# Performance work log

Measured on AMD Instinct MI355X. Metric: run time of the kernel, lower is better.

The kernel has to match this reference:

```python
import jax, jax.numpy as jnp
import numpy as np

N_HEAD = 16
ROPE_BASE = 10000.0


def _rope_tables(T, head_dim, dtype):
    inv_freq = 1.0 / (ROPE_BASE ** (jnp.arange(0, head_dim, 2, dtype=jnp.float32) / head_dim))
    t = jnp.arange(T, dtype=jnp.float32)
    freqs = t[:, None] * inv_freq[None, :]          # [T, hd/2]
    emb = jnp.concatenate([freqs, freqs], axis=-1)  # [T, hd]
    return jnp.cos(emb).astype(dtype), jnp.sin(emb).astype(dtype)


def _rotate_half(x):
    h = x.shape[-1] // 2
    return jnp.concatenate([-x[..., h:], x[..., :h]], axis=-1)


def setup_inputs() -> dict:
    key = jax.random.key(0)
    k1, k2, k3 = jax.random.split(key, 3)
    B, T, C = 2, 2048, 1024
    x = jax.random.normal(k1, (B, T, C), dtype=jnp.float32)
    w_attn = jax.random.normal(k2, (3 * C, C), dtype=jnp.float32) * (1.0 / np.sqrt(C))
    w_proj = jax.random.normal(k3, (C, C), dtype=jnp.float32) * (1.0 / np.sqrt(C))
    return {"x": x, "w_attn": w_attn, "w_proj": w_proj}


def reference(x, w_attn, w_proj):
    B, T, C = x.shape
    H = N_HEAD
    hd = C // H

    qkv = jnp.einsum('btc,fc->btf', x, w_attn)          # [B,T,3C]
    q, k, v = jnp.split(qkv, 3, axis=-1)
    # [B,H,T,hd]
    q = q.reshape(B, T, H, hd).transpose(0, 2, 1, 3)
    k = k.reshape(B, T, H, hd).transpose(0, 2, 1, 3)
    v = v.reshape(B, T, H, hd).transpose(0, 2, 1, 3)

    cos, sin = _rope_tables(T, hd, x.dtype)             # [T,hd]
    cos = cos[None, None]
    sin = sin[None, None]
    q = q * cos + _rotate_half(q) * sin
    k = k * cos + _rotate_half(k) * sin

    scale = 1.0 / np.sqrt(hd)
    scores = jnp.einsum('bhqd,bhkd->bhqk', q, k) * scale  # [B,H,T,T]
    causal = jnp.tril(jnp.ones((T, T), dtype=bool))
    scores = jnp.where(causal[None, None], scores, jnp.finfo(scores.dtype).min)
    attn = jax.nn.softmax(scores, axis=-1)
    out = jnp.einsum('bhqk,bhkd->bhqd', attn, v)          # [B,H,T,hd]
    out = out.transpose(0, 2, 1, 3).reshape(B, T, C)
    return jnp.einsum('btc,oc->bto', out, w_proj)
```

## Files before the change

### kernel.cpp

```cpp
#include <hip/hip_runtime.h>
#include <hip/hip_bf16.h>
#include <stdint.h>

typedef unsigned short u16;
typedef __bf16 bf16x8 __attribute__((ext_vector_type(8)));
typedef float f32x4 __attribute__((ext_vector_type(4)));

#define B_ 2
#define T_ 2048
#define C_ 1024
#define H_ 16
#define HD 64
#define M_ (B_ * T_)
#define N3 (3 * C_)

#define WAITV(N) asm volatile("s_waitcnt vmcnt(" #N ")" ::: "memory")

__device__ __forceinline__ float bf2f(u16 u) {
  return __uint_as_float(((unsigned int)u) << 16);
}
__device__ __forceinline__ u16 f2bf(float f) {
  unsigned int u = __float_as_uint(f);
  u += 0x7FFF + ((u >> 16) & 1);
  return (u16)(u >> 16);
}
__device__ __forceinline__ unsigned cvt_pk_bf16(float lo, float hi) {
  unsigned r;
  asm("v_cvt_pk_bf16_f32 %0, %1, %2" : "=v"(r) : "v"(lo), "v"(hi));
  return r;
}
__device__ __forceinline__ void async16(void* ldsp, const void* gp) {
  __builtin_amdgcn_global_load_lds(
      (const __attribute__((address_space(1))) unsigned int*)gp,
      (__attribute__((address_space(3))) unsigned int*)ldsp, 16, 0, 0);
}

union U16x8 { uint4 v; u16 u[8]; };

__device__ __forceinline__ bf16x8 ldsAfrag(const char* base, int row, int kbyte) {
  int off = (row * 128 + kbyte) ^ ((row & 7) << 4);
  uint4 t = *reinterpret_cast<const uint4*>(base + off);
  return __builtin_bit_cast(bf16x8, t);
}
__device__ __forceinline__ bf16x8 ldsRead(const char* p) {
  uint4 t = *reinterpret_cast<const uint4*>(p);
  return __builtin_bit_cast(bf16x8, t);
}

__global__ void cvt_bf16(const float* __restrict__ src, u16* __restrict__ dst, int n4) {
  int i = blockIdx.x * blockDim.x + threadIdx.x;
  int stride = gridDim.x * blockDim.x;
  for (; i < n4; i += stride) {
    float4 v = reinterpret_cast<const float4*>(src)[i];
    uint2 o;
    o.x = (unsigned)f2bf(v.x) | ((unsigned)f2bf(v.y) << 16);
    o.y = (unsigned)f2bf(v.z) | ((unsigned)f2bf(v.w) << 16);
    reinterpret_cast<uint2*>(dst)[i] = o;
  }
}

__global__ void rope_tables_kernel(float* __restrict__ cosT, float* __restrict__ sinT) {
  int t = blockIdx.x;
  int i = threadIdx.x;
  float inv = powf(10000.0f, -(float)i * (1.0f / 32.0f));
  float f = (float)t * inv;
  cosT[t * 32 + i] = cosf(f);
  sinT[t * 32 + i] = sinf(f);
}

template <bool OUT_F32>
__global__ __launch_bounds__(256) void gemm_bt(const u16* __restrict__ A,
                                               const u16* __restrict__ Bw,
                                               void* __restrict__ Cout,
                                               int M, int N, int K) {
  __shared__ uint4 ldsbuf[2048];
  char* As = (char*)ldsbuf;
  char* Bs = (char*)ldsbuf + 16384;
  const int tid = threadIdx.x;
  const int lane = tid & 63;
  const int wv = tid >> 6;
  const int wr = wv >> 1, wc = wv & 1;
  const int lrow = lane & 15, lgrp = lane >> 4;
  const long m0 = (long)blockIdx.x * 128, n0 = (long)blockIdx.y * 128;
  const int srow_l = lane >> 3;
  const int csrc = ((lane & 7) ^ (lane >> 3)) * 8;
  f32x4 acc[4][4] = {};
  for (int k0 = 0; k0 < K; k0 += 64) {
    __syncthreads();
#pragma unroll
    for (int p = 0; p < 4; ++p) {
      int seg = wv * 4 + p;
      int row = seg * 8 + srow_l;
      async16(As + seg * 1024, A + (size_t)(m0 + row) * K + k0 + csrc);
      async16(Bs + seg * 1024, Bw + (size_t)(n0 + row) * K + k0 + csrc);
    }
    __syncthreads();
#pragma unroll
    for (int ks = 0; ks < 2; ++ks) {
      bf16x8 af[4], bfr[4];
#pragma unroll
      for (int i = 0; i < 4; ++i) {
        af[i]  = ldsAfrag(As, wr * 64 + i * 16 + lrow, ks * 64 + lgrp * 16);
        bfr[i] = ldsAfrag(Bs, wc * 64 + i * 16 + lrow, ks * 64 + lgrp * 16);
      }
#pragma unroll
      for (int i = 0; i < 4; ++i)
#pragma unroll
        for (int j = 0; j < 4; ++j)
          acc[i][j] = __builtin_amdgcn_mfma_f32_16x16x32_bf16(af[i], bfr[j], acc[i][j], 0, 0, 0);
    }
  }
#pragma unroll
  for (int i = 0; i < 4; ++i)
#pragma unroll
    for (int j = 0; j < 4; ++j) {
      long r0 = m0 + wr * 64 + i * 16 + lgrp * 4;
      long c  = n0 + wc * 64 + j * 16 + lrow;
#pragma unroll
      for (int r = 0; r < 4; ++r) {
        float v = acc[i][j][r];
        if (OUT_F32)
          ((float*)Cout)[(r0 + r) * N + c] = v;
        else
          ((u16*)Cout)[(r0 + r) * N + c] = f2bf(v);
      }
    }
}

__global__ __launch_bounds__(256) void rope_reshape(const u16* __restrict__ qkv,
                                                    const float* __restrict__ cosT,
                                                    const float* __restrict__ sinT,
                                                    u16* __restrict__ Q,
                                                    u16* __restrict__ K,
                                                    u16* __restrict__ Vt) {
  __shared__ u16 Vs[64][80];
  const float SCLQ = 0.125f * 1.4426950408889634f;
  const int tid = threadIdx.x;
  const int tblk = blockIdx.x, bh = blockIdx.y;
  const int b = bh >> 4, h = bh & 15;
  const int tl = tid >> 2, quar = tid & 3;
  const int t = tblk * 64 + tl;
  const u16* rowp = qkv + ((size_t)(b * T_ + t)) * N3 + h * HD;
  const int d0 = quar * 8;
  float cs[8], sn[8];
#pragma unroll
  for (int j = 0; j < 8; ++j) {
    cs[j] = cosT[t * 32 + d0 + j];
    sn[j] = sinT[t * 32 + d0 + j];
  }
#pragma unroll
  for (int part = 0; part < 2; ++part) {
    const u16* p = rowp + part * C_;
    U16x8 x1, x2, o1, o2;
    x1.v = *reinterpret_cast<const uint4*>(p + d0);
    x2.v = *reinterpret_cast<const uint4*>(p + d0 + 32);
#pragma unroll
    for (int j = 0; j < 8; ++j) {
      float a = bf2f(x1.u[j]), c2 = bf2f(x2.u[j]);
      float f1 = a * cs[j] - c2 * sn[j];
      float f2 = c2 * cs[j] + a * sn[j];
      if (part == 0) { f1 *= SCLQ; f2 *= SCLQ; }
      o1.u[j] = f2bf(f1);
      o2.u[j] = f2bf(f2);
    }
    u16* dst = (part ? K : Q) + ((size_t)bh * T_ + t) * HD;
    *reinterpret_cast<uint4*>(dst + d0) = o1.v;
    *reinterpret_cast<uint4*>(dst + d0 + 32) = o2.v;
  }
  const u16* pv = rowp + 2 * C_;
#pragma unroll
  for (int c = 0; c < 2; ++c) {
    int d = quar * 16 + c * 8;
    *reinterpret_cast<uint4*>(&Vs[tl][d]) = *reinterpret_cast<const uint4*>(pv + d);
  }
  __syncthreads();
  const int d = tid >> 2, tq = tid & 3;
  U16x8 a, bv;
#pragma unroll
  for (int j = 0; j < 8; ++j) a.u[j] = Vs[tq * 16 + j][d];
#pragma unroll
  for (int j = 0; j < 8; ++j) bv.u[j] = Vs[tq * 16 + 8 + j][d];
  u16* dstv = Vt + ((size_t)bh * HD + d) * T_ + tblk * 64 + tq * 16;
  *reinterpret_cast<uint4*>(dstv) = a.v;
  *reinterpret_cast<uint4*>(dstv + 8) = bv.v;
}

__global__ __launch_bounds__(256) void attn_fwd9(const u16* __restrict__ Q,
                                                 const u16* __restrict__ K,
                                                 const u16* __restrict__ Vt,
                                                 u16* __restrict__ O) {
  __shared__ uint4 lds4[4608];
  char* ldsb = (char*)lds4;
  const int tid = threadIdx.x;
  const int lane = tid & 63, wv = tid >> 6;
  const int lrow = lane & 15, lgrp = lane >> 4;
  const int bh = blockIdx.y;
  const int b = bh >> 4, h = bh & 15;
  const u16* Qh = Q + (size_t)bh * T_ * HD;
  const u16* Kh = K + (size_t)bh * T_ * HD;
  const u16* Vh = Vt + (size_t)bh * HD * T_;

  const int srow_l = lane >> 3;
  const int csrc = ((lane & 7) ^ (lane >> 3)) * 8;

  auto stage = [&](int slot, int kt) {
    char* Kd = ldsb + (slot << 14);
    char* Vd = Kd + 8192;
    const u16* Kg = Kh + (size_t)(kt * 64) * HD;
    const u16* Vg = Vh + kt * 64;
#pragma unroll
    for (int seg = 0; seg < 2; ++seg) {
      int row = wv * 16 + seg * 8 + srow_l;
      async16(Kd + wv * 2048 + seg * 1024, Kg + (size_t)row * HD + csrc);
      async16(Vd + wv * 2048 + seg * 1024, Vg + (size_t)row * T_ + csrc);
    }
  };

  const int swz = (lrow & 7) << 4;
  const int krA = lrow * 128 + ((lgrp * 16) ^ swz);
  const int krB = lrow * 128 + ((64 + lgrp * 16) ^ swz);
  const int vrA = 8192 + krA;
  const int vrB = 8192 + krB;
  char* PsW = ldsb + 65536 + wv * 2048 + lrow * 128;
  char* pw0 = PsW + ((0 * 32 + lgrp * 8) ^ swz);
  char* pw1 = PsW + ((1 * 32 + lgrp * 8) ^ swz);
  char* pw2 = PsW + ((2 * 32 + lgrp * 8) ^ swz);
  char* pw3 = PsW + ((3 * 32 + lgrp * 8) ^ swz);
  const char* paA = PsW + ((lgrp * 16) ^ swz);
  const char* paB = PsW + ((64 + lgrp * 16) ^ swz);

  uint4 ones4;
  ones4.x = ones4.y = ones4.z = ones4.w = 0x3F803F80u;
  const bf16x8 ones8 = __builtin_bit_cast(bf16x8, ones4);

#pragma unroll
  for (int uu = 0; uu < 2; ++uu) {
    const int unit = uu ? (31 - (int)blockIdx.x) : (int)blockIdx.x;
    const int qs = unit * 64;
    const int q_glob = qs + wv * 16 + lrow;
    const int nu = unit + 1;

    bf16x8 qf[2];
#pragma unroll
    for (int ks = 0; ks < 2; ++ks) {
      uint4 t4 = *reinterpret_cast<const uint4*>(
          Qh + (size_t)(qs + wv * 16 + lrow) * HD + ks * 32 + lgrp * 8);
      qf[ks] = __builtin_bit_cast(bf16x8, t4);
    }
    f32x4 o[4] = {};
    f32x4 lacc = {};

    {
      const int pre = nu < 3 ? nu : 3;
      for (int i = 0; i < pre; ++i) stage(i, i);
      WAITV(0);
      __builtin_amdgcn_s_barrier();
      __builtin_amdgcn_sched_barrier(0);
    }

    for (int kt = 0; kt < nu; ++kt) {
      if (kt + 3 < nu) stage((kt + 3) & 3, kt + 3);
      const char* buf = ldsb + ((kt & 3) << 14);
      const char* KbA = buf + krA;
      const char* KbB = buf + krB;
      const char* VbA = buf + vrA;
      const char* VbB = buf + vrB;

      f32x4 s[4] = {};
      __builtin_amdgcn_s_setprio(1);
#pragma unroll
      for (int n = 0; n < 4; ++n)
        s[n] = __builtin_amdgcn_mfma_f32_16x16x32_bf16(ldsRead(KbA + n * 2048), qf[0], s[n], 0, 0, 0);
#pragma unroll
      for (int n = 0; n < 4; ++n)
        s[n] = __builtin_amdgcn_mfma_f32_16x16x32_bf16(ldsRead(KbB + n * 2048), qf[1], s[n], 0, 0, 0);
      __builtin_amdgcn_s_setprio(0);

      if (kt == nu - 1) {
#pragma unroll
        for (int n = 0; n < 4; ++n)
#pragma unroll
          for (int r = 0; r < 4; ++r) {
            int kg = kt * 64 + n * 16 + lgrp * 4 + r;
            float v = (kg <= q_glob) ? s[n][r] : -__builtin_inff();
            s[n][r] = exp2f(v);
          }
      } else {
#pragma unroll
        for (int n = 0; n < 4; ++n)
#pragma unroll
          for (int r = 0; r < 4; ++r) s[n][r] = exp2f(s[n][r]);
      }

      {
        uint2 w0, w1, w2, w3;
        w0.x = cvt_pk_bf16(s[0][0], s[0][1]); w0.y = cvt_pk_bf16(s[0][2], s[0][3]);
        w1.x = cvt_pk_bf16(s[1][0], s[1][1]); w1.y = cvt_pk_bf16(s[1][2], s[1][3]);
        w2.x = cvt_pk_bf16(s[2][0], s[2][1]); w2.y = cvt_pk_bf16(s[2][2], s[2][3]);
        w3.x = cvt_pk_bf16(s[3][0], s[3][1]); w3.y = cvt_pk_bf16(s[3][2], s[3][3]);
        *reinterpret_cast<uint2*>(pw0) = w0;
        *reinterpret_cast<uint2*>(pw1) = w1;
        *reinterpret_cast<uint2*>(pw2) = w2;
        *reinterpret_cast<uint2*>(pw3) = w3;
      }

      __builtin_amdgcn_s_setprio(1);
#pragma unroll
      for (int ks = 0; ks < 2; ++ks) {
        bf16x8 pa = ldsRead(ks ? paB : paA);
        lacc = __builtin_amdgcn_mfma_f32_16x16x32_bf16(pa, ones8, lacc, 0, 0, 0);
        const char* vbb = ks ? VbB : VbA;
#pragma unroll
        for (int dn = 0; dn < 4; ++dn) {
          bf16x8 bv = ldsRead(vbb + dn * 2048);
          o[dn] = __builtin_amdgcn_mfma_f32_16x16x32_bf16(pa, bv, o[dn], 0, 0, 0);
        }
      }
      __builtin_amdgcn_s_setprio(0);

      if (kt + 4 <= nu)      WAITV(8);
      else if (kt + 3 == nu) WAITV(4);
      else                   WAITV(0);
      __builtin_amdgcn_s_barrier();
      __builtin_amdgcn_sched_barrier(0);
    }

#pragma unroll
    for (int r = 0; r < 4; ++r) {
      float inv = 1.0f / lacc[r];
      int t = qs + wv * 16 + lgrp * 4 + r;
#pragma unroll
      for (int dn = 0; dn < 4; ++dn) {
        int c = h * HD + dn * 16 + lrow;
        O[((size_t)(b * T_ + t)) * C_ + c] = f2bf(o[dn][r] * inv);
      }
    }
  }
}

extern "C" void kernel_launch(void* const* d_in, const int* in_sizes, int n_in,
                              void* d_out, int out_size, void* d_ws, size_t ws_size,
                              hipStream_t stream) {
  const float* x  = (const float*)d_in[0];
  const float* wa = (const float*)d_in[1];
  const float* wp = (const float*)d_in[2];
  float* out = (float*)d_out;
  char* ws = (char*)d_ws;
  size_t off = 0;
  auto alloc = [&](size_t bytes) {
    char* p = ws + off;
    off += (bytes + 255) & ~(size_t)255;
    return p;
  };
  u16* xb   = (u16*)alloc((size_t)M_ * C_ * 2);
  u16* wab  = (u16*)alloc((size_t)N3 * C_ * 2);
  u16* wpb  = (u16*)alloc((size_t)C_ * C_ * 2);
  u16* qkvb = (u16*)alloc((size_t)M_ * N3 * 2);
  u16* Qb   = (u16*)alloc((size_t)B_ * H_ * T_ * HD * 2);
  u16* Kb   = (u16*)alloc((size_t)B_ * H_ * T_ * HD * 2);
  u16* Vtb  = (u16*)alloc((size_t)B_ * H_ * T_ * HD * 2);
  u16* Ob   = (u16*)alloc((size_t)M_ * C_ * 2);
  float* cosT = (float*)alloc((size_t)T_ * 32 * 4);
  float* sinT = (float*)alloc((size_t)T_ * 32 * 4);
  (void)in_sizes; (void)n_in; (void)out_size; (void)ws_size;

  cvt_bf16<<<1024, 256, 0, stream>>>(x, xb, M_ * C_ / 4);
  cvt_bf16<<<1024, 256, 0, stream>>>(wa, wab, N3 * C_ / 4);
  cvt_bf16<<<512, 256, 0, stream>>>(wp, wpb, C_ * C_ / 4);
  rope_tables_kernel<<<T_, 32, 0, stream>>>(cosT, sinT);
  gemm_bt<false><<<dim3(M_ / 128, N3 / 128), 256, 0, stream>>>(xb, wab, qkvb, M_, N3, C_);
  rope_reshape<<<dim3(T_ / 64, B_ * H_), 256, 0, stream>>>(qkvb, cosT, sinT, Qb, Kb, Vtb);
  attn_fwd9<<<dim3(16, B_ * H_), 256, 0, stream>>>(Qb, Kb, Vtb, Ob);
  gemm_bt<true><<<dim3(M_ / 128, C_ / 128), 256, 0, stream>>>(Ob, wpb, out, M_, C_, C_);
}
```

Baseline: 128.7 us.

## Read K/V fragments directly from global memory in attention, one q-tile per block

```diff
diff --git a/kernel.cpp b/kernel.cpp
--- a/kernel.cpp
+++ b/kernel.cpp
@@ -14,8 +14,6 @@
 #define M_ (B_ * T_)
 #define N3 (3 * C_)
 
-#define WAITV(N) asm volatile("s_waitcnt vmcnt(" #N ")" ::: "memory")
-
 __device__ __forceinline__ float bf2f(u16 u) {
   return __uint_as_float(((unsigned int)u) << 16);
 }
@@ -43,6 +41,10 @@
   return __builtin_bit_cast(bf16x8, t);
 }
 __device__ __forceinline__ bf16x8 ldsRead(const char* p) {
+  uint4 t = *reinterpret_cast<const uint4*>(p);
+  return __builtin_bit_cast(bf16x8, t);
+}
+__device__ __forceinline__ bf16x8 gRead(const char* p) {
   uint4 t = *reinterpret_cast<const uint4*>(p);
   return __builtin_bit_cast(bf16x8, t);
 }
@@ -185,43 +187,25 @@
   *reinterpret_cast<uint4*>(dstv + 8) = bv.v;
 }
 
-__global__ __launch_bounds__(256) void attn_fwd9(const u16* __restrict__ Q,
-                                                 const u16* __restrict__ K,
-                                                 const u16* __restrict__ Vt,
-                                                 u16* __restrict__ O) {
-  __shared__ uint4 lds4[4608];
-  char* ldsb = (char*)lds4;
+__global__ __launch_bounds__(256) void attn_fwd10(const u16* __restrict__ Q,
+                                                  const u16* __restrict__ K,
+                                                  const u16* __restrict__ Vt,
+                                                  u16* __restrict__ O) {
+  __shared__ char Plds[8192];
   const int tid = threadIdx.x;
   const int lane = tid & 63, wv = tid >> 6;
   const int lrow = lane & 15, lgrp = lane >> 4;
   const int bh = blockIdx.y;
   const int b = bh >> 4, h = bh & 15;
   const u16* Qh = Q + (size_t)bh * T_ * HD;
-  const u16* Kh = K + (size_t)bh * T_ * HD;
-  const u16* Vh = Vt + (size_t)bh * HD * T_;
-
-  const int srow_l = lane >> 3;
-  const int csrc = ((lane & 7) ^ (lane >> 3)) * 8;
-
-  auto stage = [&](int slot, int kt) {
-    char* Kd = ldsb + (slot << 14);
-    char* Vd = Kd + 8192;
-    const u16* Kg = Kh + (size_t)(kt * 64) * HD;
-    const u16* Vg = Vh + kt * 64;
-#pragma unroll
-    for (int seg = 0; seg < 2; ++seg) {
-      int row = wv * 16 + seg * 8 + srow_l;
-      async16(Kd + wv * 2048 + seg * 1024, Kg + (size_t)row * HD + csrc);
-      async16(Vd + wv * 2048 + seg * 1024, Vg + (size_t)row * T_ + csrc);
-    }
-  };
+  const char* Kb = (const char*)(K + (size_t)bh * T_ * HD);
+  const char* Vb = (const char*)(Vt + (size_t)bh * HD * T_);
+
+  const char* kbase = Kb + lrow * 128 + lgrp * 16;
+  const char* vbase = Vb + lrow * 4096 + lgrp * 16;
 
   const int swz = (lrow & 7) << 4;
-  const int krA = lrow * 128 + ((lgrp * 16) ^ swz);
-  const int krB = lrow * 128 + ((64 + lgrp * 16) ^ swz);
-  const int vrA = 8192 + krA;
-  const int vrB = 8192 + krB;
-  char* PsW = ldsb + 65536 + wv * 2048 + lrow * 128;
+  char* PsW = Plds + wv * 2048 + lrow * 128;
   char* pw0 = PsW + ((0 * 32 + lgrp * 8) ^ swz);
   char* pw1 = PsW + ((1 * 32 + lgrp * 8) ^ swz);
   char* pw2 = PsW + ((2 * 32 + lgrp * 8) ^ swz);
@@ -233,107 +217,86 @@
   ones4.x = ones4.y = ones4.z = ones4.w = 0x3F803F80u;
   const bf16x8 ones8 = __builtin_bit_cast(bf16x8, ones4);
 
-#pragma unroll
-  for (int uu = 0; uu < 2; ++uu) {
-    const int unit = uu ? (31 - (int)blockIdx.x) : (int)blockIdx.x;
-    const int qs = unit * 64;
-    const int q_glob = qs + wv * 16 + lrow;
-    const int nu = unit + 1;
-
-    bf16x8 qf[2];
+  const int unit = 31 - (int)blockIdx.x;
+  const int qs = unit * 64;
+  const int q_glob = qs + wv * 16 + lrow;
+  const int nu = unit + 1;
+
+  bf16x8 qf[2];
+#pragma unroll
+  for (int ks = 0; ks < 2; ++ks) {
+    uint4 t4 = *reinterpret_cast<const uint4*>(
+        Qh + (size_t)(qs + wv * 16 + lrow) * HD + ks * 32 + lgrp * 8);
+    qf[ks] = __builtin_bit_cast(bf16x8, t4);
+  }
+  f32x4 o[4] = {};
+  f32x4 lacc = {};
+
+  for (int kt = 0; kt < nu; ++kt) {
+    const char* kp = kbase + (size_t)kt * 8192;
+
+    f32x4 s[4] = {};
+    __builtin_amdgcn_s_setprio(1);
+#pragma unroll
+    for (int n = 0; n < 4; ++n) {
+      bf16x8 f0 = gRead(kp + n * 2048);
+      bf16x8 f1 = gRead(kp + n * 2048 + 64);
+      s[n] = __builtin_amdgcn_mfma_f32_16x16x32_bf16(f0, qf[0], s[n], 0, 0, 0);
+      s[n] = __builtin_amdgcn_mfma_f32_16x16x32_bf16(f1, qf[1], s[n], 0, 0, 0);
+    }
+    __builtin_amdgcn_s_setprio(0);
+
+    if (kt == nu - 1) {
+#pragma unroll
+      for (int n = 0; n < 4; ++n)
+#pragma unroll
+        for (int r = 0; r < 4; ++r) {
+          int kg = kt * 64 + n * 16 + lgrp * 4 + r;
+          float v = (kg <= q_glob) ? s[n][r] : -__builtin_inff();
+          s[n][r] = exp2f(v);
+        }
+    } else {
+#pragma unroll
+      for (int n = 0; n < 4; ++n)
+#pragma unroll
+        for (int r = 0; r < 4; ++r) s[n][r] = exp2f(s[n][r]);
+    }
+
+    {
+      uint2 w0, w1, w2, w3;
+      w0.x = cvt_pk_bf16(s[0][0], s[0][1]); w0.y = cvt_pk_bf16(s[0][2], s[0][3]);
+      w1.x = cvt_pk_bf16(s[1][0], s[1][1]); w1.y = cvt_pk_bf16(s[1][2], s[1][3]);
+      w2.x = cvt_pk_bf16(s[2][0], s[2][1]); w2.y = cvt_pk_bf16(s[2][2], s[2][3]);
+      w3.x = cvt_pk_bf16(s[3][0], s[3][1]); w3.y = cvt_pk_bf16(s[3][2], s[3][3]);
+      *reinterpret_cast<uint2*>(pw0) = w0;
+      *reinterpret_cast<uint2*>(pw1) = w1;
+      *reinterpret_cast<uint2*>(pw2) = w2;
+      *reinterpret_cast<uint2*>(pw3) = w3;
+    }
+
+    const char* vp = vbase + (size_t)kt * 128;
+    __builtin_amdgcn_s_setprio(1);
 #pragma unroll
     for (int ks = 0; ks < 2; ++ks) {
-      uint4 t4 = *reinterpret_cast<const uint4*>(
-          Qh + (size_t)(qs + wv * 16 + lrow) * HD + ks * 32 + lgrp * 8);
-      qf[ks] = __builtin_bit_cast(bf16x8, t4);
-    }
-    f32x4 o[4] = {};
-    f32x4 lacc = {};
-
-    {
-      const int pre = nu < 3 ? nu : 3;
-      for (int i = 0; i < pre; ++i) stage(i, i);
-      WAITV(0);
-      __builtin_amdgcn_s_barrier();
-      __builtin_amdgcn_sched_barrier(0);
-    }
-
-    for (int kt = 0; kt < nu; ++kt) {
-      if (kt + 3 < nu) stage((kt + 3) & 3, kt + 3);
-      const char* buf = ldsb + ((kt & 3) << 14);
-      const char* KbA = buf + krA;
-      const char* KbB = buf + krB;
-      const char* VbA = buf + vrA;
-      const char* VbB = buf + vrB;
-
-      f32x4 s[4] = {};
-      __builtin_amdgcn_s_setprio(1);
-#pragma unroll
-      for (int n = 0; n < 4; ++n)
-        s[n] = __builtin_amdgcn_mfma_f32_16x16x32_bf16(ldsRead(KbA + n * 2048), qf[0], s[n], 0, 0, 0);
-#pragma unroll
-      for (int n = 0; n < 4; ++n)
-        s[n] = __builtin_amdgcn_mfma_f32_16x16x32_bf16(ldsRead(KbB + n * 2048), qf[1], s[n], 0, 0, 0);
-      __builtin_amdgcn_s_setprio(0);
-
-      if (kt == nu - 1) {
-#pragma unroll
-        for (int n = 0; n < 4; ++n)
-#pragma unroll
-          for (int r = 0; r < 4; ++r) {
-            int kg = kt * 64 + n * 16 + lgrp * 4 + r;
-            float v = (kg <= q_glob) ? s[n][r] : -__builtin_inff();
-            s[n][r] = exp2f(v);
-          }
-      } else {
-#pragma unroll
-        for (int n = 0; n < 4; ++n)
-#pragma unroll
-          for (int r = 0; r < 4; ++r) s[n][r] = exp2f(s[n][r]);
+      bf16x8 pa = ldsRead(ks ? paB : paA);
+      lacc = __builtin_amdgcn_mfma_f32_16x16x32_bf16(pa, ones8, lacc, 0, 0, 0);
+#pragma unroll
+      for (int dn = 0; dn < 4; ++dn) {
+        bf16x8 bv = gRead(vp + dn * 65536 + ks * 64);
+        o[dn] = __builtin_amdgcn_mfma_f32_16x16x32_bf16(pa, bv, o[dn], 0, 0, 0);
       }
-
-      {
-        uint2 w0, w1, w2, w3;
-        w0.x = cvt_pk_bf16(s[0][0], s[0][1]); w0.y = cvt_pk_bf16(s[0][2], s[0][3]);
-        w1.x = cvt_pk_bf16(s[1][0], s[1][1]); w1.y = cvt_pk_bf16(s[1][2], s[1][3]);
-        w2.x = cvt_pk_bf16(s[2][0], s[2][1]); w2.y = cvt_pk_bf16(s[2][2], s[2][3]);
-        w3.x = cvt_pk_bf16(s[3][0], s[3][1]); w3.y = cvt_pk_bf16(s[3][2], s[3][3]);
-        *reinterpret_cast<uint2*>(pw0) = w0;
-        *reinterpret_cast<uint2*>(pw1) = w1;
-        *reinterpret_cast<uint2*>(pw2) = w2;
-        *reinterpret_cast<uint2*>(pw3) = w3;
-      }
-
-      __builtin_amdgcn_s_setprio(1);
-#pragma unroll
-      for (int ks = 0; ks < 2; ++ks) {
-        bf16x8 pa = ldsRead(ks ? paB : paA);
-        lacc = __builtin_amdgcn_mfma_f32_16x16x32_bf16(pa, ones8, lacc, 0, 0, 0);
-        const char* vbb = ks ? VbB : VbA;
-#pragma unroll
-        for (int dn = 0; dn < 4; ++dn) {
-          bf16x8 bv = ldsRead(vbb + dn * 2048);
-          o[dn] = __builtin_amdgcn_mfma_f32_16x16x32_bf16(pa, bv, o[dn], 0, 0, 0);
-        }
-      }
-      __builtin_amdgcn_s_setprio(0);
-
-      if (kt + 4 <= nu)      WAITV(8);
-      else if (kt + 3 == nu) WAITV(4);
-      else                   WAITV(0);
-      __builtin_amdgcn_s_barrier();
-      __builtin_amdgcn_sched_barrier(0);
-    }
-
-#pragma unroll
-    for (int r = 0; r < 4; ++r) {
-      float inv = 1.0f / lacc[r];
-      int t = qs + wv * 16 + lgrp * 4 + r;
-#pragma unroll
-      for (int dn = 0; dn < 4; ++dn) {
-        int c = h * HD + dn * 16 + lrow;
-        O[((size_t)(b * T_ + t)) * C_ + c] = f2bf(o[dn][r] * inv);
-      }
+    }
+    __builtin_amdgcn_s_setprio(0);
+  }
+
+#pragma unroll
+  for (int r = 0; r < 4; ++r) {
+    float inv = 1.0f / lacc[r];
+    int t = qs + wv * 16 + lgrp * 4 + r;
+#pragma unroll
+    for (int dn = 0; dn < 4; ++dn) {
+      int c = h * HD + dn * 16 + lrow;
+      O[((size_t)(b * T_ + t)) * C_ + c] = f2bf(o[dn][r] * inv);
     }
   }
 }
@@ -370,6 +333,6 @@
   rope_tables_kernel<<<T_, 32, 0, stream>>>(cosT, sinT);
   gemm_bt<false><<<dim3(M_ / 128, N3 / 128), 256, 0, stream>>>(xb, wab, qkvb, M_, N3, C_);
   rope_reshape<<<dim3(T_ / 64, B_ * H_), 256, 0, stream>>>(qkvb, cosT, sinT, Qb, Kb, Vtb);
-  attn_fwd9<<<dim3(16, B_ * H_), 256, 0, stream>>>(Qb, Kb, Vtb, Ob);
+  attn_fwd10<<<dim3(32, B_ * H_), 256, 0, stream>>>(Qb, Kb, Vtb, Ob);
   gemm_bt<true><<<dim3(M_ / 128, C_ / 128), 256, 0, stream>>>(Ob, wpb, out, M_, C_, C_);
 }
```

Result: slower. 304.8 us (+136.8%).

## Split paired causal units into separate blocks with double-buffered LDS staging

Applied to the files above, without the earlier changes.

```diff
diff --git a/kernel.cpp b/kernel.cpp
--- a/kernel.cpp
+++ b/kernel.cpp
@@ -13,8 +13,6 @@
 #define HD 64
 #define M_ (B_ * T_)
 #define N3 (3 * C_)
-
-#define WAITV(N) asm volatile("s_waitcnt vmcnt(" #N ")" ::: "memory")
 
 __device__ __forceinline__ float bf2f(u16 u) {
   return __uint_as_float(((unsigned int)u) << 16);
@@ -185,11 +183,11 @@
   *reinterpret_cast<uint4*>(dstv + 8) = bv.v;
 }
 
-__global__ __launch_bounds__(256) void attn_fwd9(const u16* __restrict__ Q,
-                                                 const u16* __restrict__ K,
-                                                 const u16* __restrict__ Vt,
-                                                 u16* __restrict__ O) {
-  __shared__ uint4 lds4[4608];
+__global__ __launch_bounds__(256) void attn_fwd11(const u16* __restrict__ Q,
+                                                  const u16* __restrict__ K,
+                                                  const u16* __restrict__ Vt,
+                                                  u16* __restrict__ O) {
+  __shared__ uint4 lds4[2560];
   char* ldsb = (char*)lds4;
   const int tid = threadIdx.x;
   const int lane = tid & 63, wv = tid >> 6;
@@ -221,7 +219,7 @@
   const int krB = lrow * 128 + ((64 + lgrp * 16) ^ swz);
   const int vrA = 8192 + krA;
   const int vrB = 8192 + krB;
-  char* PsW = ldsb + 65536 + wv * 2048 + lrow * 128;
+  char* PsW = ldsb + 32768 + wv * 2048 + lrow * 128;
   char* pw0 = PsW + ((0 * 32 + lgrp * 8) ^ swz);
   char* pw1 = PsW + ((1 * 32 + lgrp * 8) ^ swz);
   char* pw2 = PsW + ((2 * 32 + lgrp * 8) ^ swz);
@@ -233,107 +231,96 @@
   ones4.x = ones4.y = ones4.z = ones4.w = 0x3F803F80u;
   const bf16x8 ones8 = __builtin_bit_cast(bf16x8, ones4);
 
-#pragma unroll
-  for (int uu = 0; uu < 2; ++uu) {
-    const int unit = uu ? (31 - (int)blockIdx.x) : (int)blockIdx.x;
-    const int qs = unit * 64;
-    const int q_glob = qs + wv * 16 + lrow;
-    const int nu = unit + 1;
-
-    bf16x8 qf[2];
+  const int unit = 31 - (int)blockIdx.x;
+  const int qs = unit * 64;
+  const int q_glob = qs + wv * 16 + lrow;
+  const int nu = unit + 1;
+
+  bf16x8 qf[2];
+#pragma unroll
+  for (int ks = 0; ks < 2; ++ks) {
+    uint4 t4 = *reinterpret_cast<const uint4*>(
+        Qh + (size_t)(qs + wv * 16 + lrow) * HD + ks * 32 + lgrp * 8);
+    qf[ks] = __builtin_bit_cast(bf16x8, t4);
+  }
+  f32x4 o[4] = {};
+  f32x4 lacc = {};
+
+  stage(0, 0);
+  __syncthreads();
+
+  int cur = 0;
+  for (int kt = 0; kt < nu; ++kt) {
+    if (kt + 1 < nu) stage(cur ^ 1, kt + 1);
+    const char* buf = ldsb + (cur << 14);
+    const char* KbA = buf + krA;
+    const char* KbB = buf + krB;
+    const char* VbA = buf + vrA;
+    const char* VbB = buf + vrB;
+
+    f32x4 s[4] = {};
+    __builtin_amdgcn_s_setprio(1);
+#pragma unroll
+    for (int n = 0; n < 4; ++n)
+      s[n] = __builtin_amdgcn_mfma_f32_16x16x32_bf16(ldsRead(KbA + n * 2048), qf[0], s[n], 0, 0, 0);
+#pragma unroll
+    for (int n = 0; n < 4; ++n)
+      s[n] = __builtin_amdgcn_mfma_f32_16x16x32_bf16(ldsRead(KbB + n * 2048), qf[1], s[n], 0, 0, 0);
+    __builtin_amdgcn_s_setprio(0);
+
+    if (kt == nu - 1) {
+#pragma unroll
+      for (int n = 0; n < 4; ++n)
+#pragma unroll
+        for (int r = 0; r < 4; ++r) {
+          int kg = kt * 64 + n * 16 + lgrp * 4 + r;
+          float v = (kg <= q_glob) ? s[n][r] : -__builtin_inff();
+          s[n][r] = exp2f(v);
+        }
+    } else {
+#pragma unroll
+      for (int n = 0; n < 4; ++n)
+#pragma unroll
+        for (int r = 0; r < 4; ++r) s[n][r] = exp2f(s[n][r]);
+    }
+
+    {
+      uint2 w0, w1, w2, w3;
+      w0.x = cvt_pk_bf16(s[0][0], s[0][1]); w0.y = cvt_pk_bf16(s[0][2], s[0][3]);
+      w1.x = cvt_pk_bf16(s[1][0], s[1][1]); w1.y = cvt_pk_bf16(s[1][2], s[1][3]);
+      w2.x = cvt_pk_bf16(s[2][0], s[2][1]); w2.y = cvt_pk_bf16(s[2][2], s[2][3]);
+      w3.x = cvt_pk_bf16(s[3][0], s[3][1]); w3.y = cvt_pk_bf16(s[3][2], s[3][3]);
+      *reinterpret_cast<uint2*>(pw0) = w0;
+      *reinterpret_cast<uint2*>(pw1) = w1;
+      *reinterpret_cast<uint2*>(pw2) = w2;
+      *reinterpret_cast<uint2*>(pw3) = w3;
+    }
+
+    __builtin_amdgcn_s_setprio(1);
 #pragma unroll
     for (int ks = 0; ks < 2; ++ks) {
-      uint4 t4 = *reinterpret_cast<const uint4*>(
-          Qh + (size_t)(qs + wv * 16 + lrow) * HD + ks * 32 + lgrp * 8);
-      qf[ks] = __builtin_bit_cast(bf16x8, t4);
-    }
-    f32x4 o[4] = {};
-    f32x4 lacc = {};
-
-    {
-      const int pre = nu < 3 ? nu : 3;
-      for (int i = 0; i < pre; ++i) stage(i, i);
-      WAITV(0);
-      __builtin_amdgcn_s_barrier();
-      __builtin_amdgcn_sched_barrier(0);
-    }
-
-    for (int kt = 0; kt < nu; ++kt) {
-      if (kt + 3 < nu) stage((kt + 3) & 3, kt + 3);
-      const char* buf = ldsb + ((kt & 3) << 14);
-      const char* KbA = buf + krA;
-      const char* KbB = buf + krB;
-      const char* VbA = buf + vrA;
-      const char* VbB = buf + vrB;
-
-      f32x4 s[4] = {};
-      __builtin_amdgcn_s_setprio(1);
-#pragma unroll
-      for (int n = 0; n < 4; ++n)
-        s[n] = __builtin_amdgcn_mfma_f32_16x16x32_bf16(ldsRead(KbA + n * 2048), qf[0], s[n], 0, 0, 0);
-#pragma unroll
-      for (int n = 0; n < 4; ++n)
-        s[n] = __builtin_amdgcn_mfma_f32_16x16x32_bf16(ldsRead(KbB + n * 2048), qf[1], s[n], 0, 0, 0);
-      __builtin_amdgcn_s_setprio(0);
-
-      if (kt == nu - 1) {
-#pragma unroll
-        for (int n = 0; n < 4; ++n)
-#pragma unroll
-          for (int r = 0; r < 4; ++r) {
-            int kg = kt * 64 + n * 16 + lgrp * 4 + r;
-            float v = (kg <= q_glob) ? s[n][r] : -__builtin_inff();
-            s[n][r] = exp2f(v);
-          }
-      } else {
-#pragma unroll
-        for (int n = 0; n < 4; ++n)
-#pragma unroll
-          for (int r = 0; r < 4; ++r) s[n][r] = exp2f(s[n][r]);
+      bf16x8 pa = ldsRead(ks ? paB : paA);
+      lacc = __builtin_amdgcn_mfma_f32_16x16x32_bf16(pa, ones8, lacc, 0, 0, 0);
+      const char* vbb = ks ? VbB : VbA;
+#pragma unroll
+      for (int dn = 0; dn < 4; ++dn) {
+        bf16x8 bv = ldsRead(vbb + dn * 2048);
+        o[dn] = __builtin_amdgcn_mfma_f32_16x16x32_bf16(pa, bv, o[dn], 0, 0, 0);
       }
-
-      {
-        uint2 w0, w1, w2, w3;
-        w0.x = cvt_pk_bf16(s[0][0], s[0][1]); w0.y = cvt_pk_bf16(s[0][2], s[0][3]);
-        w1.x = cvt_pk_bf16(s[1][0], s[1][1]); w1.y = cvt_pk_bf16(s[1][2], s[1][3]);
-        w2.x = cvt_pk_bf16(s[2][0], s[2][1]); w2.y = cvt_pk_bf16(s[2][2], s[2][3]);
-        w3.x = cvt_pk_bf16(s[3][0], s[3][1]); w3.y = cvt_pk_bf16(s[3][2], s[3][3]);
-        *reinterpret_cast<uint2*>(pw0) = w0;
-        *reinterpret_cast<uint2*>(pw1) = w1;
-        *reinterpret_cast<uint2*>(pw2) = w2;
-        *reinterpret_cast<uint2*>(pw3) = w3;
-      }
-
-      __builtin_amdgcn_s_setprio(1);
-#pragma unroll
-      for (int ks = 0; ks < 2; ++ks) {
-        bf16x8 pa = ldsRead(ks ? paB : paA);
-        lacc = __builtin_amdgcn_mfma_f32_16x16x32_bf16(pa, ones8, lacc, 0, 0, 0);
-        const char* vbb = ks ? VbB : VbA;
-#pragma unroll
-        for (int dn = 0; dn < 4; ++dn) {
-          bf16x8 bv = ldsRead(vbb + dn * 2048);
-          o[dn] = __builtin_amdgcn_mfma_f32_16x16x32_bf16(pa, bv, o[dn], 0, 0, 0);
-        }
-      }
-      __builtin_amdgcn_s_setprio(0);
-
-      if (kt + 4 <= nu)      WAITV(8);
-      else if (kt + 3 == nu) WAITV(4);
-      else                   WAITV(0);
-      __builtin_amdgcn_s_barrier();
-      __builtin_amdgcn_sched_barrier(0);
-    }
-
-#pragma unroll
-    for (int r = 0; r < 4; ++r) {
-      float inv = 1.0f / lacc[r];
-      int t = qs + wv * 16 + lgrp * 4 + r;
-#pragma unroll
-      for (int dn = 0; dn < 4; ++dn) {
-        int c = h * HD + dn * 16 + lrow;
-        O[((size_t)(b * T_ + t)) * C_ + c] = f2bf(o[dn][r] * inv);
-      }
+    }
+    __builtin_amdgcn_s_setprio(0);
+    __syncthreads();
+    cur ^= 1;
+  }
+
+#pragma unroll
+  for (int r = 0; r < 4; ++r) {
+    float inv = 1.0f / lacc[r];
+    int t = qs + wv * 16 + lgrp * 4 + r;
+#pragma unroll
+    for (int dn = 0; dn < 4; ++dn) {
+      int c = h * HD + dn * 16 + lrow;
+      O[((size_t)(b * T_ + t)) * C_ + c] = f2bf(o[dn][r] * inv);
     }
   }
 }
@@ -370,6 +357,6 @@
   rope_tables_kernel<<<T_, 32, 0, stream>>>(cosT, sinT);
   gemm_bt<false><<<dim3(M_ / 128, N3 / 128), 256, 0, stream>>>(xb, wab, qkvb, M_, N3, C_);
   rope_reshape<<<dim3(T_ / 64, B_ * H_), 256, 0, stream>>>(qkvb, cosT, sinT, Qb, Kb, Vtb);
-  attn_fwd9<<<dim3(16, B_ * H_), 256, 0, stream>>>(Qb, Kb, Vtb, Ob);
+  attn_fwd11<<<dim3(32, B_ * H_), 256, 0, stream>>>(Qb, Kb, Vtb, Ob);
   gemm_bt<true><<<dim3(M_ / 128, C_ / 128), 256, 0, stream>>>(Ob, wpb, out, M_, C_, C_);
 }
```

Measured after the change: 139.8 us. +8.6%, slower.

## Fuse RoPE into QKV GEMM epilogue and merge conversion kernels

Applied to the files above, without the earlier changes.

```diff
diff --git a/kernel.cpp b/kernel.cpp
--- a/kernel.cpp
+++ b/kernel.cpp
@@ -47,25 +47,34 @@
   return __builtin_bit_cast(bf16x8, t);
 }
 
-__global__ void cvt_bf16(const float* __restrict__ src, u16* __restrict__ dst, int n4) {
+#define NX4  (M_ * C_ / 4)
+#define NWA4 (N3 * C_ / 4)
+#define NWP4 (C_ * C_ / 4)
+#define NTOT4 (NX4 + NWA4 + NWP4)
+__global__ void cvt3(const float* __restrict__ x, const float* __restrict__ wa,
+                     const float* __restrict__ wp, u16* __restrict__ xb,
+                     u16* __restrict__ wab, u16* __restrict__ wpb) {
   int i = blockIdx.x * blockDim.x + threadIdx.x;
   int stride = gridDim.x * blockDim.x;
-  for (; i < n4; i += stride) {
-    float4 v = reinterpret_cast<const float4*>(src)[i];
+  for (; i < NTOT4; i += stride) {
+    const float* src; u16* dst; int j = i;
+    if (j < NX4) { src = x; dst = xb; }
+    else if (j < NX4 + NWA4) { j -= NX4; src = wa; dst = wab; }
+    else { j -= NX4 + NWA4; src = wp; dst = wpb; }
+    float4 v = reinterpret_cast<const float4*>(src)[j];
     uint2 o;
     o.x = (unsigned)f2bf(v.x) | ((unsigned)f2bf(v.y) << 16);
     o.y = (unsigned)f2bf(v.z) | ((unsigned)f2bf(v.w) << 16);
-    reinterpret_cast<uint2*>(dst)[i] = o;
-  }
-}
-
-__global__ void rope_tables_kernel(float* __restrict__ cosT, float* __restrict__ sinT) {
+    reinterpret_cast<uint2*>(dst)[j] = o;
+  }
+}
+
+__global__ void rope_tables_kernel(float2* __restrict__ rtab) {
   int t = blockIdx.x;
   int i = threadIdx.x;
   float inv = powf(10000.0f, -(float)i * (1.0f / 32.0f));
   float f = (float)t * inv;
-  cosT[t * 32 + i] = cosf(f);
-  sinT[t * 32 + i] = sinf(f);
+  rtab[t * 32 + i] = make_float2(cosf(f), sinf(f));
 }
 
 template <bool OUT_F32>
@@ -127,47 +136,96 @@
     }
 }
 
-__global__ __launch_bounds__(256) void rope_reshape(const u16* __restrict__ qkv,
-                                                    const float* __restrict__ cosT,
-                                                    const float* __restrict__ sinT,
-                                                    u16* __restrict__ Q,
-                                                    u16* __restrict__ K,
-                                                    u16* __restrict__ Vt) {
+__global__ __launch_bounds__(256) void gemm_qkv(const u16* __restrict__ A,
+                                                const u16* __restrict__ Bw,
+                                                const float2* __restrict__ rtab,
+                                                u16* __restrict__ Qb,
+                                                u16* __restrict__ Kb,
+                                                u16* __restrict__ vtmp) {
+  __shared__ uint4 ldsbuf[2048];
+  char* As = (char*)ldsbuf;
+  char* Bs = (char*)ldsbuf + 16384;
+  const int tid = threadIdx.x;
+  const int lane = tid & 63;
+  const int wv = tid >> 6;
+  const int wr = wv >> 1, wc = wv & 1;
+  const int lrow = lane & 15, lgrp = lane >> 4;
+  const long m0 = (long)blockIdx.x * 128, n0 = (long)blockIdx.y * 128;
+  const int srow_l = lane >> 3;
+  const int csrc = ((lane & 7) ^ (lane >> 3)) * 8;
+  f32x4 acc[4][4] = {};
+  for (int k0 = 0; k0 < C_; k0 += 64) {
+    __syncthreads();
+#pragma unroll
+    for (int p = 0; p < 4; ++p) {
+      int seg = wv * 4 + p;
+      int row = seg * 8 + srow_l;
+      async16(As + seg * 1024, A + (size_t)(m0 + row) * C_ + k0 + csrc);
+      async16(Bs + seg * 1024, Bw + (size_t)(n0 + row) * C_ + k0 + csrc);
+    }
+    __syncthreads();
+#pragma unroll
+    for (int ks = 0; ks < 2; ++ks) {
+      bf16x8 af[4], bfr[4];
+#pragma unroll
+      for (int i = 0; i < 4; ++i) {
+        af[i]  = ldsAfrag(As, wr * 64 + i * 16 + lrow, ks * 64 + lgrp * 16);
+        bfr[i] = ldsAfrag(Bs, wc * 64 + i * 16 + lrow, ks * 64 + lgrp * 16);
+      }
+#pragma unroll
+      for (int i = 0; i < 4; ++i)
+#pragma unroll
+        for (int j = 0; j < 4; ++j)
+          acc[i][j] = __builtin_amdgcn_mfma_f32_16x16x32_bf16(af[i], bfr[j], acc[i][j], 0, 0, 0);
+    }
+  }
+  const float SCLQ = 0.125f * 1.4426950408889634f;
+  if (n0 < 2048) {
+    u16* dst = (n0 < 1024) ? Qb : Kb;
+    const float scl = (n0 < 1024) ? SCLQ : 1.0f;
+    const int cb = ((int)n0 & 1023) + wc * 64;
+    const int h = cb >> 6;
+#pragma unroll
+    for (int i = 0; i < 4; ++i)
+#pragma unroll
+      for (int r = 0; r < 4; ++r) {
+        int grow = (int)m0 + wr * 64 + i * 16 + lgrp * 4 + r;
+        int b = grow >> 11, t = grow & 2047;
+        const float2* rt = rtab + t * 32;
+        size_t base = ((size_t)((b * 16 + h) * 2048 + t)) * 64;
+#pragma unroll
+        for (int j = 0; j < 2; ++j) {
+          int d = j * 16 + lrow;
+          float2 cn = rt[d];
+          float lo = acc[i][j][r], hi = acc[i][j + 2][r];
+          dst[base + d]      = f2bf((lo * cn.x - hi * cn.y) * scl);
+          dst[base + d + 32] = f2bf((hi * cn.x + lo * cn.y) * scl);
+        }
+      }
+  } else {
+    const int cb = (int)n0 - 2048 + wc * 64;
+#pragma unroll
+    for (int i = 0; i < 4; ++i)
+#pragma unroll
+      for (int j = 0; j < 4; ++j) {
+        int c = cb + j * 16 + lrow;
+        long r0 = m0 + wr * 64 + i * 16 + lgrp * 4;
+#pragma unroll
+        for (int r = 0; r < 4; ++r)
+          vtmp[(r0 + r) * 1024 + c] = f2bf(acc[i][j][r]);
+      }
+  }
+}
+
+__global__ __launch_bounds__(256) void v_transpose(const u16* __restrict__ vtmp,
+                                                   u16* __restrict__ Vt) {
   __shared__ u16 Vs[64][80];
-  const float SCLQ = 0.125f * 1.4426950408889634f;
   const int tid = threadIdx.x;
   const int tblk = blockIdx.x, bh = blockIdx.y;
   const int b = bh >> 4, h = bh & 15;
   const int tl = tid >> 2, quar = tid & 3;
   const int t = tblk * 64 + tl;
-  const u16* rowp = qkv + ((size_t)(b * T_ + t)) * N3 + h * HD;
-  const int d0 = quar * 8;
-  float cs[8], sn[8];
-#pragma unroll
-  for (int j = 0; j < 8; ++j) {
-    cs[j] = cosT[t * 32 + d0 + j];
-    sn[j] = sinT[t * 32 + d0 + j];
-  }
-#pragma unroll
-  for (int part = 0; part < 2; ++part) {
-    const u16* p = rowp + part * C_;
-    U16x8 x1, x2, o1, o2;
-    x1.v = *reinterpret_cast<const uint4*>(p + d0);
-    x2.v = *reinterpret_cast<const uint4*>(p + d0 + 32);
-#pragma unroll
-    for (int j = 0; j < 8; ++j) {
-      float a = bf2f(x1.u[j]), c2 = bf2f(x2.u[j]);
-      float f1 = a * cs[j] - c2 * sn[j];
-      float f2 = c2 * cs[j] + a * sn[j];
-      if (part == 0) { f1 *= SCLQ; f2 *= SCLQ; }
-      o1.u[j] = f2bf(f1);
-      o2.u[j] = f2bf(f2);
-    }
-    u16* dst = (part ? K : Q) + ((size_t)bh * T_ + t) * HD;
-    *reinterpret_cast<uint4*>(dst + d0) = o1.v;
-    *reinterpret_cast<uint4*>(dst + d0 + 32) = o2.v;
-  }
-  const u16* pv = rowp + 2 * C_;
+  const u16* pv = vtmp + ((size_t)(b * T_ + t)) * C_ + h * HD;
 #pragma unroll
   for (int c = 0; c < 2; ++c) {
     int d = quar * 16 + c * 8;
@@ -355,21 +413,18 @@
   u16* xb   = (u16*)alloc((size_t)M_ * C_ * 2);
   u16* wab  = (u16*)alloc((size_t)N3 * C_ * 2);
   u16* wpb  = (u16*)alloc((size_t)C_ * C_ * 2);
-  u16* qkvb = (u16*)alloc((size_t)M_ * N3 * 2);
+  u16* vtmp = (u16*)alloc((size_t)M_ * C_ * 2);
   u16* Qb   = (u16*)alloc((size_t)B_ * H_ * T_ * HD * 2);
   u16* Kb   = (u16*)alloc((size_t)B_ * H_ * T_ * HD * 2);
   u16* Vtb  = (u16*)alloc((size_t)B_ * H_ * T_ * HD * 2);
   u16* Ob   = (u16*)alloc((size_t)M_ * C_ * 2);
-  float* cosT = (float*)alloc((size_t)T_ * 32 * 4);
-  float* sinT = (float*)alloc((size_t)T_ * 32 * 4);
+  float2* rtab = (float2*)alloc((size_t)T_ * 32 * 8);
   (void)in_sizes; (void)n_in; (void)out_size; (void)ws_size;
 
-  cvt_bf16<<<1024, 256, 0, stream>>>(x, xb, M_ * C_ / 4);
-  cvt_bf16<<<1024, 256, 0, stream>>>(wa, wab, N3 * C_ / 4);
-  cvt_bf16<<<512, 256, 0, stream>>>(wp, wpb, C_ * C_ / 4);
-  rope_tables_kernel<<<T_, 32, 0, stream>>>(cosT, sinT);
-  gemm_bt<false><<<dim3(M_ / 128, N3 / 128), 256, 0, stream>>>(xb, wab, qkvb, M_, N3, C_);
-  rope_reshape<<<dim3(T_ / 64, B_ * H_), 256, 0, stream>>>(qkvb, cosT, sinT, Qb, Kb, Vtb);
+  cvt3<<<2048, 256, 0, stream>>>(x, wa, wp, xb, wab, wpb);
+  rope_tables_kernel<<<T_, 32, 0, stream>>>(rtab);
+  gemm_qkv<<<dim3(M_ / 128, N3 / 128), 256, 0, stream>>>(xb, wab, rtab, Qb, Kb, vtmp);
+  v_transpose<<<dim3(T_ / 64, B_ * H_), 256, 0, stream>>>(vtmp, Vtb);
   attn_fwd9<<<dim3(16, B_ * H_), 256, 0, stream>>>(Qb, Kb, Vtb, Ob);
   gemm_bt<true><<<dim3(M_ / 128, C_ / 128), 256, 0, stream>>>(Ob, wpb, out, M_, C_, C_);
 }
```

Result: slower. 133.6 us (+3.8%).
